# Optimization experiments

Hardware: AMD Instinct MI355X
Metric: run time of the kernel (lower is better)

The kernel has to match this reference:

```python
import jax, jax.numpy as jnp
import numpy as np
from jax import lax

VOCAB = 100000; E = 512; HID = 1024; H = HID // 2; T = 7; L = 4096
START = 4; STOP = 5; NEG = -10000.0


def setup_inputs() -> dict:
    key = jax.random.key(0)
    ks = jax.random.split(key, 14)
    s = 0.05  # ~1/sqrt(H), matches torch default init scale
    transitions = jax.random.normal(ks[12], (T, T), dtype=jnp.float32)
    transitions = transitions.at[START, :].set(NEG).at[:, STOP].set(NEG)
    return {
        "sentence": jax.random.randint(ks[0], (L,), 0, VOCAB),
        "emb": jax.random.normal(ks[1], (VOCAB, E), dtype=jnp.float32) * s,
        "w_ih_f": jax.random.normal(ks[2], (4 * H, E), dtype=jnp.float32) * s,
        "w_hh_f": jax.random.normal(ks[3], (4 * H, H), dtype=jnp.float32) * s,
        "b_ih_f": jax.random.normal(ks[4], (4 * H,), dtype=jnp.float32) * s,
        "b_hh_f": jax.random.normal(ks[5], (4 * H,), dtype=jnp.float32) * s,
        "w_ih_b": jax.random.normal(ks[6], (4 * H, E), dtype=jnp.float32) * s,
        "w_hh_b": jax.random.normal(ks[7], (4 * H, H), dtype=jnp.float32) * s,
        "b_ih_b": jax.random.normal(ks[8], (4 * H,), dtype=jnp.float32) * s,
        "b_hh_b": jax.random.normal(ks[9], (4 * H,), dtype=jnp.float32) * s,
        "w_out": jax.random.normal(ks[10], (T, HID), dtype=jnp.float32) * s,
        "b_out": jax.random.normal(ks[11], (T,), dtype=jnp.float32) * s,
        "transitions": transitions,
    }


def _lstm_dir(x, w_ih, w_hh, b_ih, b_hh):
    # x: [L, E] -> hidden states [L, H]; zero initial state (torch default)
    xg = x @ w_ih.T + b_ih  # [L, 4H] precomputed input gates
    h0 = jnp.zeros((H,), x.dtype)
    c0 = jnp.zeros((H,), x.dtype)
    def step(carry, g):
        h, c = carry
        gates = g + w_hh @ h + b_hh
        i, f, gg, o = jnp.split(gates, 4)
        i = jax.nn.sigmoid(i); f = jax.nn.sigmoid(f)
        gg = jnp.tanh(gg); o = jax.nn.sigmoid(o)
        c = f * c + i * gg
        h = o * jnp.tanh(c)
        return (h, c), h
    _, hs = lax.scan(step, (h0, c0), xg)
    return hs


def reference(sentence, emb, w_ih_f, w_hh_f, b_ih_f, b_hh_f,
              w_ih_b, w_hh_b, b_ih_b, b_hh_b, w_out, b_out, transitions):
    x = emb[sentence]  # [L, E]
    hf = _lstm_dir(x, w_ih_f, w_hh_f, b_ih_f, b_hh_f)            # [L, H]
    hb = _lstm_dir(x[::-1], w_ih_b, w_hh_b, b_ih_b, b_hh_b)[::-1]
    feats = jnp.concatenate([hf, hb], axis=1) @ w_out.T + b_out  # [L, T]

    # Viterbi max-plus DP
    init = jnp.full((T,), NEG, feats.dtype).at[START].set(0.0)
    def vstep(fv, feat):
        sc = fv[None, :] + transitions           # [next, prev]
        bp = jnp.argmax(sc, axis=1)
        return jnp.max(sc, axis=1) + feat, bp
    fv, bptrs = lax.scan(vstep, init, feats)     # bptrs: [L, T]
    terminal = fv + transitions[STOP]
    best = jnp.argmax(terminal)
    score = terminal[best]
    # backtrack
    def bt(tag, bp):
        return bp[tag], tag
    _, path_rev = lax.scan(bt, best, bptrs[::-1])
    best_path = path_rev[::-1]                   # [L] tag ids
    return best_path, score
```

## Files before the change

kernel.cpp:

```cpp
#include <hip/hip_runtime.h>
#include <hip/hip_bf16.h>

#define L     4096
#define E     512
#define HID   1024
#define HH    512
#define G4    2048
#define T_TAG 7
#define START_TAG 4
#define STOP_TAG  5
#define NEGV  (-10000.0f)

#define NBLK  16
#define SENT  0xFFFFFFFFu

__global__ __launch_bounds__(256)
void xg_kernel(const int* __restrict__ sentence, const float* __restrict__ emb,
               const float* __restrict__ wih_f, const float* __restrict__ bih_f,
               const float* __restrict__ bhh_f,
               const float* __restrict__ wih_b, const float* __restrict__ bih_b,
               const float* __restrict__ bhh_b,
               float* __restrict__ xg_f, float* __restrict__ xg_b)
{
    const int dir = blockIdx.z;
    const float* __restrict__ wih = dir ? wih_b : wih_f;
    const float* __restrict__ bih = dir ? bih_b : bih_f;
    const float* __restrict__ bhh = dir ? bhh_b : bhh_f;
    float* __restrict__ xg = dir ? xg_b : xg_f;

    const int t0 = blockIdx.x * 64;
    const int j0 = blockIdx.y * 64;

    __shared__ float As[32][68];
    __shared__ float Bs[32][68];
    __shared__ int   sent[64];

    const int tid = threadIdx.x;
    if (tid < 64) sent[tid] = sentence[t0 + tid];
    __syncthreads();

    const int tx = tid & 15;
    const int ty = tid >> 4;

    float acc[4][4];
#pragma unroll
    for (int a = 0; a < 4; a++)
#pragma unroll
        for (int b = 0; b < 4; b++) acc[a][b] = 0.f;

    for (int k0 = 0; k0 < E; k0 += 32) {
        __syncthreads();
#pragma unroll
        for (int q = 0; q < 2; q++) {
            const int f  = q * 256 + tid;
            const int i  = f >> 3;
            const int k4 = (f & 7) * 4;
            const float4 av = *(const float4*)(emb + (size_t)sent[i] * E + k0 + k4);
            As[k4 + 0][i] = av.x; As[k4 + 1][i] = av.y;
            As[k4 + 2][i] = av.z; As[k4 + 3][i] = av.w;
            const float4 bv = *(const float4*)(wih + (size_t)(j0 + i) * E + k0 + k4);
            Bs[k4 + 0][i] = bv.x; Bs[k4 + 1][i] = bv.y;
            Bs[k4 + 2][i] = bv.z; Bs[k4 + 3][i] = bv.w;
        }
        __syncthreads();
#pragma unroll
        for (int k = 0; k < 32; k++) {
            const float4 a4 = *(const float4*)&As[k][ty * 4];
            const float4 b4 = *(const float4*)&Bs[k][tx * 4];
            const float a[4] = { a4.x, a4.y, a4.z, a4.w };
            const float b[4] = { b4.x, b4.y, b4.z, b4.w };
#pragma unroll
            for (int ii = 0; ii < 4; ii++)
#pragma unroll
                for (int jj = 0; jj < 4; jj++) acc[ii][jj] += a[ii] * b[jj];
        }
    }

#pragma unroll
    for (int ii = 0; ii < 4; ii++) {
        const int t = t0 + ty * 4 + ii;
#pragma unroll
        for (int jj = 0; jj < 4; jj++) {
            const int j = j0 + tx * 4 + jj;
            xg[(size_t)t * G4 + j] = acc[ii][jj] + bih[j] + bhh[j];
        }
    }
}

__global__ __launch_bounds__(512)
void lstm_kernel(const float* __restrict__ xg_f, const float* __restrict__ xg_b,
                 const float* __restrict__ whh_f, const float* __restrict__ whh_b,
                 float* __restrict__ hf, float* __restrict__ hb)
{
    const int dir = blockIdx.x >> 4;
    const int rnk = blockIdx.x & 15;

    const float* __restrict__ xg  = dir ? xg_b  : xg_f;
    const float* __restrict__ whh = dir ? whh_b : whh_f;
    float* __restrict__ hout = dir ? hb : hf;

    const int tid  = threadIdx.x;
    const int wave = tid >> 6;
    const int lane = tid & 63;
    const int g    = wave >> 1;
    const int jh   = wave & 1;
    const int u0   = rnk * 32;

    float w[16][8];
#pragma unroll
    for (int rr = 0; rr < 16; rr++) {
        const size_t row = (size_t)(g * HH + u0 + jh * 16 + rr);
#pragma unroll
        for (int k = 0; k < 8; k++)
            w[rr][k] = whh[row * HH + (size_t)(k * 64 + lane)];
    }

    __shared__ float h_lds[2][HH];
    __shared__ float glds[8][16];
    float c_state = 0.f;
    const int uu = u0 + (tid & 31);

    float xq0 = 0.f, xq1 = 0.f, xq2 = 0.f, xq3 = 0.f;
    if (tid < 32) {
        const float* xgt = xg + (size_t)(dir ? (L - 1) : 0) * G4;
        xq0 = xgt[uu];            xq1 = xgt[HH + uu];
        xq2 = xgt[2 * HH + uu];   xq3 = xgt[3 * HH + uu];
    }

    for (int s = 0; s < L; s++) {
        const int t = dir ? (L - 1 - s) : s;
        const int p = s & 1;

        unsigned int v = 0;
        if (s > 0) {
            const int tp = dir ? (t + 1) : (t - 1);
            const unsigned int* hp =
                (const unsigned int*)(hout + (size_t)tp * HH) + tid;
            do {
                v = __hip_atomic_load(hp, __ATOMIC_RELAXED,
                                      __HIP_MEMORY_SCOPE_AGENT);
            } while (v == SENT);
        }
        h_lds[p][tid] = __uint_as_float(v);
        __syncthreads();

        float hv[8];
#pragma unroll
        for (int k = 0; k < 8; k++) hv[k] = h_lds[p][k * 64 + lane];

        float acc[16];
#pragma unroll
        for (int rr = 0; rr < 16; rr++) {
            float a = 0.f;
#pragma unroll
            for (int k = 0; k < 8; k++) a += w[rr][k] * hv[k];
            acc[rr] = a;
        }

        {
            const bool b0 = lane & 1;
#pragma unroll
            for (int r = 0; r < 8; r++) {
                const float send = b0 ? acc[r] : acc[r + 8];
                const float recv = __shfl_xor(send, 1, 64);
                acc[r] = (b0 ? acc[r + 8] : acc[r]) + recv;
            }
            const bool b1 = lane & 2;
#pragma unroll
            for (int r = 0; r < 4; r++) {
                const float send = b1 ? acc[r] : acc[r + 4];
                const float recv = __shfl_xor(send, 2, 64);
                acc[r] = (b1 ? acc[r + 4] : acc[r]) + recv;
            }
            const bool b2 = lane & 4;
#pragma unroll
            for (int r = 0; r < 2; r++) {
                const float send = b2 ? acc[r] : acc[r + 2];
                const float recv = __shfl_xor(send, 4, 64);
                acc[r] = (b2 ? acc[r + 2] : acc[r]) + recv;
            }
            const bool b3 = lane & 8;
            {
                const float send = b3 ? acc[0] : acc[1];
                const float recv = __shfl_xor(send, 8, 64);
                acc[0] = (b3 ? acc[1] : acc[0]) + recv;
            }
            acc[0] += __shfl_xor(acc[0], 16, 64);
            acc[0] += __shfl_xor(acc[0], 32, 64);
        }
        if (lane < 16) {
            const int R = ((lane & 1) << 3) | ((lane & 2) << 1) |
                          ((lane & 4) >> 1) | ((lane & 8) >> 3);
            glds[wave][R] = acc[0];
        }
        __syncthreads();

        if (tid < 32) {
            const int j   = tid;
            const int jh_ = j >> 4;
            const int rr  = j & 15;
            float iv = glds[0 + jh_][rr] + xq0;
            float fv = glds[2 + jh_][rr] + xq1;
            float gv = glds[4 + jh_][rr] + xq2;
            float ov = glds[6 + jh_][rr] + xq3;
            iv = 1.f / (1.f + expf(-iv));
            fv = 1.f / (1.f + expf(-fv));
            gv = tanhf(gv);
            ov = 1.f / (1.f + expf(-ov));
            c_state = fv * c_state + iv * gv;
            const float hval = ov * tanhf(c_state);
            __hip_atomic_store((unsigned int*)&hout[(size_t)t * HH + uu],
                               __float_as_uint(hval), __ATOMIC_RELAXED,
                               __HIP_MEMORY_SCOPE_AGENT);
            if (s + 1 < L) {
                const int tn = dir ? (t - 1) : (t + 1);
                const float* xgt = xg + (size_t)tn * G4;
                xq0 = xgt[uu];            xq1 = xgt[HH + uu];
                xq2 = xgt[2 * HH + uu];   xq3 = xgt[3 * HH + uu];
            }
        }
    }
}

__global__ __launch_bounds__(256)
void feats_kernel(const float* __restrict__ hf, const float* __restrict__ hb,
                  const float* __restrict__ wout, const float* __restrict__ bout,
                  float* __restrict__ feats)
{
    const int t   = blockIdx.x;
    const int tid = threadIdx.x;

    float acc[T_TAG];
#pragma unroll
    for (int i = 0; i < T_TAG; i++) acc[i] = 0.f;

    for (int c = tid; c < HID; c += 256) {
        const float v = (c < HH) ? hf[(size_t)t * HH + c]
                                 : hb[(size_t)t * HH + (c - HH)];
#pragma unroll
        for (int i = 0; i < T_TAG; i++) acc[i] += v * wout[i * HID + c];
    }
#pragma unroll
    for (int m = 1; m < 64; m <<= 1) {
#pragma unroll
        for (int i = 0; i < T_TAG; i++) acc[i] += __shfl_xor(acc[i], m, 64);
    }

    __shared__ float red[4][T_TAG];
    const int wave = tid >> 6, lane = tid & 63;
    if (lane == 0) {
#pragma unroll
        for (int i = 0; i < T_TAG; i++) red[wave][i] = acc[i];
    }
    __syncthreads();
    if (tid < T_TAG) {
        feats[(size_t)t * 8 + tid] =
            red[0][tid] + red[1][tid] + red[2][tid] + red[3][tid] + bout[tid];
    }
}

__global__ __launch_bounds__(64)
void viterbi_kernel(const float* __restrict__ feats, const float* __restrict__ trans,
                    float* __restrict__ out)
{
    __shared__ unsigned char bp[L][T_TAG];

    const int tid = threadIdx.x;
    const int i = tid >> 3, j = tid & 7;
    const bool valid = (i < T_TAG) && (j < T_TAG);
    const float trij = valid ? trans[i * T_TAG + j] : -1e30f;

    float fv;
    if (j < T_TAG) fv = (j == START_TAG) ? 0.f : NEGV;
    else           fv = -1e30f;

    const int ieff = (i < T_TAG) ? i : 0;
    float fq[8];
#pragma unroll
    for (int p = 0; p < 8; p++) fq[p] = feats[(size_t)p * 8 + ieff];

    for (int t = 0; t < L; t++) {
        const float sc = fv + trij;
        float best = sc; int bj = j;
#pragma unroll
        for (int m = 1; m < 8; m <<= 1) {
            const float ov = __shfl_xor(best, m, 8);
            const int   oj = __shfl_xor(bj, m, 8);
            if (ov > best || (ov == best && oj < bj)) { best = ov; bj = oj; }
        }
        const float f_t = fq[t & 7];
        if (t + 8 < L) fq[t & 7] = feats[(size_t)(t + 8) * 8 + ieff];
        const float fvnew = best + f_t;
        if (valid && j == 0) bp[t][i] = (unsigned char)bj;
        const float nf = __shfl(fvnew, (j < T_TAG) ? j * 8 : 0, 64);
        fv = (j < T_TAG) ? nf : -1e30f;
    }

    float term = fv + ((j < T_TAG) ? trans[STOP_TAG * T_TAG + j] : -1e30f);
    float bestt = term; int bt = j;
#pragma unroll
    for (int m = 1; m < 8; m <<= 1) {
        const float ov = __shfl_xor(bestt, m, 8);
        const int   oj = __shfl_xor(bt, m, 8);
        if (ov > bestt || (ov == bestt && oj < bt)) { bestt = ov; bt = oj; }
    }

    if (tid == 0) {
        out[L] = bestt;
        int tag = bt;
        out[L - 1] = (float)tag;
        for (int t = L - 1; t >= 1; t--) {
            tag = bp[t][tag];
            out[t - 1] = (float)tag;
        }
    }
}

extern "C" void kernel_launch(void* const* d_in, const int* in_sizes, int n_in,
                              void* d_out, int out_size, void* d_ws, size_t ws_size,
                              hipStream_t stream)
{
    const int*   sentence = (const int*)  d_in[0];
    const float* emb      = (const float*)d_in[1];
    const float* wih_f    = (const float*)d_in[2];
    const float* whh_f    = (const float*)d_in[3];
    const float* bih_f    = (const float*)d_in[4];
    const float* bhh_f    = (const float*)d_in[5];
    const float* wih_b    = (const float*)d_in[6];
    const float* whh_b    = (const float*)d_in[7];
    const float* bih_b    = (const float*)d_in[8];
    const float* bhh_b    = (const float*)d_in[9];
    const float* wout     = (const float*)d_in[10];
    const float* bout     = (const float*)d_in[11];
    const float* trans    = (const float*)d_in[12];
    float* out = (float*)d_out;

    char* ws = (char*)d_ws;
    float* xg_f   = (float*)(ws + 1024);
    float* xg_b   = xg_f  + (size_t)L * G4;
    float* hfbuf  = xg_b  + (size_t)L * G4;
    float* hbbuf  = hfbuf + (size_t)L * HH;
    float* featsb = hbbuf + (size_t)L * HH;

    hipMemsetAsync(hfbuf, 0xFF, (size_t)2 * L * HH * sizeof(float), stream);

    hipLaunchKernelGGL(xg_kernel, dim3(L / 64, G4 / 64, 2), dim3(256), 0, stream,
                       sentence, emb, wih_f, bih_f, bhh_f, wih_b, bih_b, bhh_b,
                       xg_f, xg_b);

    void* args[] = { (void*)&xg_f, (void*)&xg_b, (void*)&whh_f, (void*)&whh_b,
                     (void*)&hfbuf, (void*)&hbbuf };
    hipLaunchCooperativeKernel((void*)lstm_kernel, dim3(2 * NBLK), dim3(512),
                               args, 0, stream);

    hipLaunchKernelGGL(feats_kernel, dim3(L), dim3(256), 0, stream,
                       hfbuf, hbbuf, wout, bout, featsb);

    hipLaunchKernelGGL(viterbi_kernel, dim3(1), dim3(64), 0, stream,
                       featsb, trans, out);
}
```

Measured before the change: 9.919 ms.

## Fuse input-gate GEMM, LSTM recurrence and feats into one pipelined cooperative kernel

Merges the input-projection GEMM, the bidirectional LSTM recurrence and the tag-feature projection into a single cooperative launch. 32 worker blocks run the recurrence while 224 helper blocks compute xg tiles in time order and publish per-chunk counters, then compute feats as hidden states appear. This hides the GEMM and feats kernels behind the serial recurrence and removes launch gaps. In exchange it adds spin-waits on counters and sentinels, and helper blocks may compete with worker blocks for memory bandwidth.

After: 9.808 ms. No clear change (-1.1%).

```diff
diff --git a/kernel.cpp b/kernel.cpp
--- a/kernel.cpp
+++ b/kernel.cpp
@@ -11,251 +11,292 @@
 #define STOP_TAG  5
 #define NEGV  (-10000.0f)
 
-#define NBLK  16
+#define NWRK  32
+#define NHELP 224
+#define NTILE (64 * 2 * 32)
 #define SENT  0xFFFFFFFFu
 
-__global__ __launch_bounds__(256)
-void xg_kernel(const int* __restrict__ sentence, const float* __restrict__ emb,
-               const float* __restrict__ wih_f, const float* __restrict__ bih_f,
-               const float* __restrict__ bhh_f,
-               const float* __restrict__ wih_b, const float* __restrict__ bih_b,
-               const float* __restrict__ bhh_b,
-               float* __restrict__ xg_f, float* __restrict__ xg_b)
+__device__ __forceinline__ float aload_f(const float* p) {
+    const unsigned int v = __hip_atomic_load((const unsigned int*)p,
+                                             __ATOMIC_RELAXED,
+                                             __HIP_MEMORY_SCOPE_AGENT);
+    return __uint_as_float(v);
+}
+__device__ __forceinline__ void astore_f(float* p, float x) {
+    __hip_atomic_store((unsigned int*)p, __float_as_uint(x),
+                       __ATOMIC_RELAXED, __HIP_MEMORY_SCOPE_AGENT);
+}
+
+__global__ __launch_bounds__(512)
+void fused_kernel(const int* __restrict__ sentence, const float* __restrict__ emb,
+                  const float* __restrict__ wih_f, const float* __restrict__ bih_f,
+                  const float* __restrict__ bhh_f,
+                  const float* __restrict__ wih_b, const float* __restrict__ bih_b,
+                  const float* __restrict__ bhh_b,
+                  const float* __restrict__ whh_f, const float* __restrict__ whh_b,
+                  const float* __restrict__ wout, const float* __restrict__ bout,
+                  float* __restrict__ xg_f, float* __restrict__ xg_b,
+                  float* __restrict__ hf, float* __restrict__ hb,
+                  float* __restrict__ feats, int* cnt)
 {
-    const int dir = blockIdx.z;
-    const float* __restrict__ wih = dir ? wih_b : wih_f;
-    const float* __restrict__ bih = dir ? bih_b : bih_f;
-    const float* __restrict__ bhh = dir ? bhh_b : bhh_f;
-    float* __restrict__ xg = dir ? xg_b : xg_f;
-
-    const int t0 = blockIdx.x * 64;
-    const int j0 = blockIdx.y * 64;
-
+    const int bid = blockIdx.x;
+    const int tid = threadIdx.x;
+
+    __shared__ float h_lds[2][HH];
+    __shared__ float glds[8][16];
     __shared__ float As[32][68];
     __shared__ float Bs[32][68];
-    __shared__ int   sent[64];
-
-    const int tid = threadIdx.x;
-    if (tid < 64) sent[tid] = sentence[t0 + tid];
-    __syncthreads();
-
-    const int tx = tid & 15;
-    const int ty = tid >> 4;
-
-    float acc[4][4];
-#pragma unroll
-    for (int a = 0; a < 4; a++)
-#pragma unroll
-        for (int b = 0; b < 4; b++) acc[a][b] = 0.f;
-
-    for (int k0 = 0; k0 < E; k0 += 32) {
+    __shared__ int   sent_s[64];
+    __shared__ float red_s[8][8];
+
+    if (bid < NWRK) {
+        const int dir = bid >> 4;
+        const int rnk = bid & 15;
+
+        const float* __restrict__ xg  = dir ? xg_b  : xg_f;
+        const float* __restrict__ whh = dir ? whh_b : whh_f;
+        float* __restrict__ hout = dir ? hb : hf;
+
+        const int wave = tid >> 6;
+        const int lane = tid & 63;
+        const int g    = wave >> 1;
+        const int jh   = wave & 1;
+        const int u0   = rnk * 32;
+
+        float w[16][8];
+#pragma unroll
+        for (int rr = 0; rr < 16; rr++) {
+            const size_t row = (size_t)(g * HH + u0 + jh * 16 + rr);
+#pragma unroll
+            for (int k = 0; k < 8; k++)
+                w[rr][k] = whh[row * HH + (size_t)(k * 64 + lane)];
+        }
+
+        float c_state = 0.f;
+        const int uu = u0 + (tid & 31);
+
+        auto wait_chunk = [&](int tc) {
+            const int* cp = cnt + dir * 64 + tc;
+            while (__hip_atomic_load(cp, __ATOMIC_ACQUIRE,
+                                     __HIP_MEMORY_SCOPE_AGENT) < 32) {
+                __builtin_amdgcn_s_sleep(1);
+            }
+        };
+
+        float xq0 = 0.f, xq1 = 0.f, xq2 = 0.f, xq3 = 0.f;
+        if (tid < 32) {
+            wait_chunk(dir ? 63 : 0);
+            const float* xgt = xg + (size_t)(dir ? (L - 1) : 0) * G4;
+            xq0 = aload_f(xgt + uu);            xq1 = aload_f(xgt + HH + uu);
+            xq2 = aload_f(xgt + 2 * HH + uu);   xq3 = aload_f(xgt + 3 * HH + uu);
+        }
+
+        for (int s = 0; s < L; s++) {
+            const int t = dir ? (L - 1 - s) : s;
+            const int p = s & 1;
+
+            unsigned int v = 0;
+            if (s > 0) {
+                const int tp = dir ? (t + 1) : (t - 1);
+                const unsigned int* hp =
+                    (const unsigned int*)(hout + (size_t)tp * HH) + tid;
+                do {
+                    v = __hip_atomic_load(hp, __ATOMIC_RELAXED,
+                                          __HIP_MEMORY_SCOPE_AGENT);
+                } while (v == SENT);
+            }
+            h_lds[p][tid] = __uint_as_float(v);
+            __syncthreads();
+
+            float hv[8];
+#pragma unroll
+            for (int k = 0; k < 8; k++) hv[k] = h_lds[p][k * 64 + lane];
+
+            float acc[16];
+#pragma unroll
+            for (int rr = 0; rr < 16; rr++) {
+                float a = 0.f;
+#pragma unroll
+                for (int k = 0; k < 8; k++) a += w[rr][k] * hv[k];
+                acc[rr] = a;
+            }
+
+            {
+                const bool b0 = lane & 1;
+#pragma unroll
+                for (int r = 0; r < 8; r++) {
+                    const float send = b0 ? acc[r] : acc[r + 8];
+                    const float recv = __shfl_xor(send, 1, 64);
+                    acc[r] = (b0 ? acc[r + 8] : acc[r]) + recv;
+                }
+                const bool b1 = lane & 2;
+#pragma unroll
+                for (int r = 0; r < 4; r++) {
+                    const float send = b1 ? acc[r] : acc[r + 4];
+                    const float recv = __shfl_xor(send, 2, 64);
+                    acc[r] = (b1 ? acc[r + 4] : acc[r]) + recv;
+                }
+                const bool b2 = lane & 4;
+#pragma unroll
+                for (int r = 0; r < 2; r++) {
+                    const float send = b2 ? acc[r] : acc[r + 2];
+                    const float recv = __shfl_xor(send, 4, 64);
+                    acc[r] = (b2 ? acc[r + 2] : acc[r]) + recv;
+                }
+                const bool b3 = lane & 8;
+                {
+                    const float send = b3 ? acc[0] : acc[1];
+                    const float recv = __shfl_xor(send, 8, 64);
+                    acc[0] = (b3 ? acc[1] : acc[0]) + recv;
+                }
+                acc[0] += __shfl_xor(acc[0], 16, 64);
+                acc[0] += __shfl_xor(acc[0], 32, 64);
+            }
+            if (lane < 16) {
+                const int R = ((lane & 1) << 3) | ((lane & 2) << 1) |
+                              ((lane & 4) >> 1) | ((lane & 8) >> 3);
+                glds[wave][R] = acc[0];
+            }
+            __syncthreads();
+
+            if (tid < 32) {
+                const int jh_ = tid >> 4;
+                const int rr  = tid & 15;
+                float iv = glds[0 + jh_][rr] + xq0;
+                float fv = glds[2 + jh_][rr] + xq1;
+                float gv = glds[4 + jh_][rr] + xq2;
+                float ov = glds[6 + jh_][rr] + xq3;
+                iv = 1.f / (1.f + expf(-iv));
+                fv = 1.f / (1.f + expf(-fv));
+                gv = tanhf(gv);
+                ov = 1.f / (1.f + expf(-ov));
+                c_state = fv * c_state + iv * gv;
+                const float hval = ov * tanhf(c_state);
+                __hip_atomic_store((unsigned int*)&hout[(size_t)t * HH + uu],
+                                   __float_as_uint(hval), __ATOMIC_RELAXED,
+                                   __HIP_MEMORY_SCOPE_AGENT);
+                if (s + 1 < L) {
+                    const int tn = dir ? (t - 1) : (t + 1);
+                    if ((tn & 63) == (dir ? 63 : 0)) wait_chunk(tn >> 6);
+                    const float* xgt = xg + (size_t)tn * G4;
+                    xq0 = aload_f(xgt + uu);
+                    xq1 = aload_f(xgt + HH + uu);
+                    xq2 = aload_f(xgt + 2 * HH + uu);
+                    xq3 = aload_f(xgt + 3 * HH + uu);
+                }
+            }
+        }
+        return;
+    }
+
+    const int hid_ = bid - NWRK;
+
+    for (int tile = hid_; tile < NTILE; tile += NHELP) {
+        const int jt = tile & 31;
+        const int sd = tile >> 5;
+        const int dr = sd & 1;
+        const int sc = sd >> 1;
+        const int t0 = dr ? (L - 64 - sc * 64) : (sc * 64);
+        const int j0 = jt * 64;
+        const float* __restrict__ wih = dr ? wih_b : wih_f;
+        const float* __restrict__ bih = dr ? bih_b : bih_f;
+        const float* __restrict__ bhh = dr ? bhh_b : bhh_f;
+        float* __restrict__ xg = dr ? xg_b : xg_f;
+
+        if (tid < 64) sent_s[tid] = sentence[t0 + tid];
+
+        const int li = tid >> 3;
+        const int k4 = (tid & 7) * 4;
+        const int tx = tid & 15;
+        const int ty = tid >> 4;
+
+        float a00 = 0.f, a01 = 0.f, a02 = 0.f, a03 = 0.f;
+        float a10 = 0.f, a11 = 0.f, a12 = 0.f, a13 = 0.f;
+
+        for (int k0 = 0; k0 < E; k0 += 32) {
+            __syncthreads();
+            {
+                const float4 av = *(const float4*)(emb + (size_t)sent_s[li] * E + k0 + k4);
+                As[k4 + 0][li] = av.x; As[k4 + 1][li] = av.y;
+                As[k4 + 2][li] = av.z; As[k4 + 3][li] = av.w;
+                const float4 bv = *(const float4*)(wih + (size_t)(j0 + li) * E + k0 + k4);
+                Bs[k4 + 0][li] = bv.x; Bs[k4 + 1][li] = bv.y;
+                Bs[k4 + 2][li] = bv.z; Bs[k4 + 3][li] = bv.w;
+            }
+            __syncthreads();
+#pragma unroll
+            for (int k = 0; k < 32; k++) {
+                const float a0 = As[k][ty * 2 + 0];
+                const float a1 = As[k][ty * 2 + 1];
+                const float4 b4 = *(const float4*)&Bs[k][tx * 4];
+                a00 += a0 * b4.x; a01 += a0 * b4.y; a02 += a0 * b4.z; a03 += a0 * b4.w;
+                a10 += a1 * b4.x; a11 += a1 * b4.y; a12 += a1 * b4.z; a13 += a1 * b4.w;
+            }
+        }
+
+        {
+            const int c0 = j0 + tx * 4;
+            const float bsum0 = bih[c0 + 0] + bhh[c0 + 0];
+            const float bsum1 = bih[c0 + 1] + bhh[c0 + 1];
+            const float bsum2 = bih[c0 + 2] + bhh[c0 + 2];
+            const float bsum3 = bih[c0 + 3] + bhh[c0 + 3];
+            float* r0 = xg + (size_t)(t0 + ty * 2 + 0) * G4 + c0;
+            float* r1 = xg + (size_t)(t0 + ty * 2 + 1) * G4 + c0;
+            astore_f(r0 + 0, a00 + bsum0); astore_f(r0 + 1, a01 + bsum1);
+            astore_f(r0 + 2, a02 + bsum2); astore_f(r0 + 3, a03 + bsum3);
+            astore_f(r1 + 0, a10 + bsum0); astore_f(r1 + 1, a11 + bsum1);
+            astore_f(r1 + 2, a12 + bsum2); astore_f(r1 + 3, a13 + bsum3);
+        }
         __syncthreads();
-#pragma unroll
-        for (int q = 0; q < 2; q++) {
-            const int f  = q * 256 + tid;
-            const int i  = f >> 3;
-            const int k4 = (f & 7) * 4;
-            const float4 av = *(const float4*)(emb + (size_t)sent[i] * E + k0 + k4);
-            As[k4 + 0][i] = av.x; As[k4 + 1][i] = av.y;
-            As[k4 + 2][i] = av.z; As[k4 + 3][i] = av.w;
-            const float4 bv = *(const float4*)(wih + (size_t)(j0 + i) * E + k0 + k4);
-            Bs[k4 + 0][i] = bv.x; Bs[k4 + 1][i] = bv.y;
-            Bs[k4 + 2][i] = bv.z; Bs[k4 + 3][i] = bv.w;
+        if (tid == 0)
+            __hip_atomic_fetch_add(&cnt[dr * 64 + (t0 >> 6)], 1,
+                                   __ATOMIC_RELEASE, __HIP_MEMORY_SCOPE_AGENT);
+    }
+
+    const int wave = tid >> 6, lane = tid & 63;
+    for (int t = hid_; t < L; t += NHELP) {
+        if (tid < 32) {
+            const float* src = (tid < 16) ? hf : hb;
+            const unsigned int* wp =
+                (const unsigned int*)(src + (size_t)t * HH) + (tid & 15) * 32;
+            while (__hip_atomic_load(wp, __ATOMIC_RELAXED,
+                                     __HIP_MEMORY_SCOPE_AGENT) == SENT) {
+                __builtin_amdgcn_s_sleep(8);
+            }
         }
         __syncthreads();
-#pragma unroll
-        for (int k = 0; k < 32; k++) {
-            const float4 a4 = *(const float4*)&As[k][ty * 4];
-            const float4 b4 = *(const float4*)&Bs[k][tx * 4];
-            const float a[4] = { a4.x, a4.y, a4.z, a4.w };
-            const float b[4] = { b4.x, b4.y, b4.z, b4.w };
-#pragma unroll
-            for (int ii = 0; ii < 4; ii++)
-#pragma unroll
-                for (int jj = 0; jj < 4; jj++) acc[ii][jj] += a[ii] * b[jj];
-        }
-    }
-
-#pragma unroll
-    for (int ii = 0; ii < 4; ii++) {
-        const int t = t0 + ty * 4 + ii;
-#pragma unroll
-        for (int jj = 0; jj < 4; jj++) {
-            const int j = j0 + tx * 4 + jj;
-            xg[(size_t)t * G4 + j] = acc[ii][jj] + bih[j] + bhh[j];
-        }
-    }
-}
-
-__global__ __launch_bounds__(512)
-void lstm_kernel(const float* __restrict__ xg_f, const float* __restrict__ xg_b,
-                 const float* __restrict__ whh_f, const float* __restrict__ whh_b,
-                 float* __restrict__ hf, float* __restrict__ hb)
-{
-    const int dir = blockIdx.x >> 4;
-    const int rnk = blockIdx.x & 15;
-
-    const float* __restrict__ xg  = dir ? xg_b  : xg_f;
-    const float* __restrict__ whh = dir ? whh_b : whh_f;
-    float* __restrict__ hout = dir ? hb : hf;
-
-    const int tid  = threadIdx.x;
-    const int wave = tid >> 6;
-    const int lane = tid & 63;
-    const int g    = wave >> 1;
-    const int jh   = wave & 1;
-    const int u0   = rnk * 32;
-
-    float w[16][8];
-#pragma unroll
-    for (int rr = 0; rr < 16; rr++) {
-        const size_t row = (size_t)(g * HH + u0 + jh * 16 + rr);
-#pragma unroll
-        for (int k = 0; k < 8; k++)
-            w[rr][k] = whh[row * HH + (size_t)(k * 64 + lane)];
-    }
-
-    __shared__ float h_lds[2][HH];
-    __shared__ float glds[8][16];
-    float c_state = 0.f;
-    const int uu = u0 + (tid & 31);
-
-    float xq0 = 0.f, xq1 = 0.f, xq2 = 0.f, xq3 = 0.f;
-    if (tid < 32) {
-        const float* xgt = xg + (size_t)(dir ? (L - 1) : 0) * G4;
-        xq0 = xgt[uu];            xq1 = xgt[HH + uu];
-        xq2 = xgt[2 * HH + uu];   xq3 = xgt[3 * HH + uu];
-    }
-
-    for (int s = 0; s < L; s++) {
-        const int t = dir ? (L - 1 - s) : s;
-        const int p = s & 1;
-
-        unsigned int v = 0;
-        if (s > 0) {
-            const int tp = dir ? (t + 1) : (t - 1);
-            const unsigned int* hp =
-                (const unsigned int*)(hout + (size_t)tp * HH) + tid;
-            do {
-                v = __hip_atomic_load(hp, __ATOMIC_RELAXED,
-                                      __HIP_MEMORY_SCOPE_AGENT);
-            } while (v == SENT);
-        }
-        h_lds[p][tid] = __uint_as_float(v);
+
+        const unsigned int* p0 = (const unsigned int*)(hf + (size_t)t * HH) + tid;
+        const unsigned int* p1 = (const unsigned int*)(hb + (size_t)t * HH) + tid;
+        unsigned int v0, v1;
+        do { v0 = __hip_atomic_load(p0, __ATOMIC_RELAXED,
+                                    __HIP_MEMORY_SCOPE_AGENT); } while (v0 == SENT);
+        do { v1 = __hip_atomic_load(p1, __ATOMIC_RELAXED,
+                                    __HIP_MEMORY_SCOPE_AGENT); } while (v1 == SENT);
+        const float x0 = __uint_as_float(v0);
+        const float x1 = __uint_as_float(v1);
+
+        float acc[T_TAG];
+#pragma unroll
+        for (int i = 0; i < T_TAG; i++)
+            acc[i] = x0 * wout[i * HID + tid] + x1 * wout[i * HID + HH + tid];
+#pragma unroll
+        for (int m = 1; m < 64; m <<= 1) {
+#pragma unroll
+            for (int i = 0; i < T_TAG; i++) acc[i] += __shfl_xor(acc[i], m, 64);
+        }
+        if (lane == 0) {
+#pragma unroll
+            for (int i = 0; i < T_TAG; i++) red_s[wave][i] = acc[i];
+        }
         __syncthreads();
-
-        float hv[8];
-#pragma unroll
-        for (int k = 0; k < 8; k++) hv[k] = h_lds[p][k * 64 + lane];
-
-        float acc[16];
-#pragma unroll
-        for (int rr = 0; rr < 16; rr++) {
-            float a = 0.f;
-#pragma unroll
-            for (int k = 0; k < 8; k++) a += w[rr][k] * hv[k];
-            acc[rr] = a;
-        }
-
-        {
-            const bool b0 = lane & 1;
-#pragma unroll
-            for (int r = 0; r < 8; r++) {
-                const float send = b0 ? acc[r] : acc[r + 8];
-                const float recv = __shfl_xor(send, 1, 64);
-                acc[r] = (b0 ? acc[r + 8] : acc[r]) + recv;
-            }
-            const bool b1 = lane & 2;
-#pragma unroll
-            for (int r = 0; r < 4; r++) {
-                const float send = b1 ? acc[r] : acc[r + 4];
-                const float recv = __shfl_xor(send, 2, 64);
-                acc[r] = (b1 ? acc[r + 4] : acc[r]) + recv;
-            }
-            const bool b2 = lane & 4;
-#pragma unroll
-            for (int r = 0; r < 2; r++) {
-                const float send = b2 ? acc[r] : acc[r + 2];
-                const float recv = __shfl_xor(send, 4, 64);
-                acc[r] = (b2 ? acc[r + 2] : acc[r]) + recv;
-            }
-            const bool b3 = lane & 8;
-            {
-                const float send = b3 ? acc[0] : acc[1];
-                const float recv = __shfl_xor(send, 8, 64);
-                acc[0] = (b3 ? acc[1] : acc[0]) + recv;
-            }
-            acc[0] += __shfl_xor(acc[0], 16, 64);
-            acc[0] += __shfl_xor(acc[0], 32, 64);
-        }
-        if (lane < 16) {
-            const int R = ((lane & 1) << 3) | ((lane & 2) << 1) |
-                          ((lane & 4) >> 1) | ((lane & 8) >> 3);
-            glds[wave][R] = acc[0];
+        if (tid < T_TAG) {
+            float ssum = bout[tid];
+#pragma unroll
+            for (int wv = 0; wv < 8; wv++) ssum += red_s[wv][tid];
+            feats[(size_t)t * 8 + tid] = ssum;
         }
         __syncthreads();
-
-        if (tid < 32) {
-            const int j   = tid;
-            const int jh_ = j >> 4;
-            const int rr  = j & 15;
-            float iv = glds[0 + jh_][rr] + xq0;
-            float fv = glds[2 + jh_][rr] + xq1;
-            float gv = glds[4 + jh_][rr] + xq2;
-            float ov = glds[6 + jh_][rr] + xq3;
-            iv = 1.f / (1.f + expf(-iv));
-            fv = 1.f / (1.f + expf(-fv));
-            gv = tanhf(gv);
-            ov = 1.f / (1.f + expf(-ov));
-            c_state = fv * c_state + iv * gv;
-            const float hval = ov * tanhf(c_state);
-            __hip_atomic_store((unsigned int*)&hout[(size_t)t * HH + uu],
-                               __float_as_uint(hval), __ATOMIC_RELAXED,
-                               __HIP_MEMORY_SCOPE_AGENT);
-            if (s + 1 < L) {
-                const int tn = dir ? (t - 1) : (t + 1);
-                const float* xgt = xg + (size_t)tn * G4;
-                xq0 = xgt[uu];            xq1 = xgt[HH + uu];
-                xq2 = xgt[2 * HH + uu];   xq3 = xgt[3 * HH + uu];
-            }
-        }
-    }
-}
-
-__global__ __launch_bounds__(256)
-void feats_kernel(const float* __restrict__ hf, const float* __restrict__ hb,
-                  const float* __restrict__ wout, const float* __restrict__ bout,
-                  float* __restrict__ feats)
-{
-    const int t   = blockIdx.x;
-    const int tid = threadIdx.x;
-
-    float acc[T_TAG];
-#pragma unroll
-    for (int i = 0; i < T_TAG; i++) acc[i] = 0.f;
-
-    for (int c = tid; c < HID; c += 256) {
-        const float v = (c < HH) ? hf[(size_t)t * HH + c]
-                                 : hb[(size_t)t * HH + (c - HH)];
-#pragma unroll
-        for (int i = 0; i < T_TAG; i++) acc[i] += v * wout[i * HID + c];
-    }
-#pragma unroll
-    for (int m = 1; m < 64; m <<= 1) {
-#pragma unroll
-        for (int i = 0; i < T_TAG; i++) acc[i] += __shfl_xor(acc[i], m, 64);
-    }
-
-    __shared__ float red[4][T_TAG];
-    const int wave = tid >> 6, lane = tid & 63;
-    if (lane == 0) {
-#pragma unroll
-        for (int i = 0; i < T_TAG; i++) red[wave][i] = acc[i];
-    }
-    __syncthreads();
-    if (tid < T_TAG) {
-        feats[(size_t)t * 8 + tid] =
-            red[0][tid] + red[1][tid] + red[2][tid] + red[3][tid] + bout[tid];
     }
 }
 
@@ -336,25 +377,26 @@
     float* out = (float*)d_out;
 
     char* ws = (char*)d_ws;
+    int*   cnt    = (int*)ws;
     float* xg_f   = (float*)(ws + 1024);
     float* xg_b   = xg_f  + (size_t)L * G4;
     float* hfbuf  = xg_b  + (size_t)L * G4;
     float* hbbuf  = hfbuf + (size_t)L * HH;
     float* featsb = hbbuf + (size_t)L * HH;
 
+    hipMemsetAsync(cnt, 0, 1024, stream);
     hipMemsetAsync(hfbuf, 0xFF, (size_t)2 * L * HH * sizeof(float), stream);
 
-    hipLaunchKernelGGL(xg_kernel, dim3(L / 64, G4 / 64, 2), dim3(256), 0, stream,
-                       sentence, emb, wih_f, bih_f, bhh_f, wih_b, bih_b, bhh_b,
-                       xg_f, xg_b);
-
-    void* args[] = { (void*)&xg_f, (void*)&xg_b, (void*)&whh_f, (void*)&whh_b,
-                     (void*)&hfbuf, (void*)&hbbuf };
-    hipLaunchCooperativeKernel((void*)lstm_kernel, dim3(2 * NBLK), dim3(512),
-                               args, 0, stream);
-
-    hipLaunchKernelGGL(feats_kernel, dim3(L), dim3(256), 0, stream,
-                       hfbuf, hbbuf, wout, bout, featsb);
+    void* args[] = { (void*)&sentence, (void*)&emb,
+                     (void*)&wih_f, (void*)&bih_f, (void*)&bhh_f,
+                     (void*)&wih_b, (void*)&bih_b, (void*)&bhh_b,
+                     (void*)&whh_f, (void*)&whh_b,
+                     (void*)&wout, (void*)&bout,
+                     (void*)&xg_f, (void*)&xg_b,
+                     (void*)&hfbuf, (void*)&hbbuf,
+                     (void*)&featsb, (void*)&cnt };
+    hipLaunchCooperativeKernel((void*)fused_kernel, dim3(NWRK + NHELP),
+                               dim3(512), args, 0, stream);
 
     hipLaunchKernelGGL(viterbi_kernel, dim3(1), dim3(64), 0, stream,
                        featsb, trans, out);
```
